# Kernel tuning notes

Measured on AMD Instinct MI355X. Metric: run time of the kernel, lower is better.

The kernel has to match this reference:

```python
import jax
import jax.numpy as jnp
from jax import lax
import numpy as np

B, T, C, L = 512, 512, 128, 80
BLANK = C - 1  # Keras ctc_batch_cost uses last class as blank
NEG = -1e30
EPS = 1e-7


def setup_inputs() -> dict:
    key = jax.random.key(0)
    k1, k2 = jax.random.split(key)
    # y_pred: positive "probability-like" activations, as ctc_batch_cost expects
    y_pred = jax.random.uniform(k1, (B, T, C), dtype=jnp.float32)
    # labels: non-blank symbols in [0, C-2]
    y_true = jax.random.randint(k2, (B, L), 0, C - 1, dtype=jnp.int64)
    return {"y_true": y_true, "y_pred": y_pred}


def _ctc_loss(log_probs, labels):
    """log_probs: [B,T,C] log-softmax; labels: [B,L] ints. Returns [B,1] loss."""
    b, t, c = log_probs.shape
    l = labels.shape[1]
    s = 2 * l + 1
    # extended label sequence: blank, l1, blank, l2, ..., blank  -> [B,S]
    ext = jnp.full((b, s), BLANK, dtype=labels.dtype).at[:, 1::2].set(labels)
    # per-time log-prob of each extended symbol: [B,T,S]
    lp = jnp.take_along_axis(log_probs, ext[:, None, :], axis=2)
    # skip-transition allowed where symbol is non-blank and differs from s-2
    ext_m2 = jnp.concatenate([jnp.full((b, 2), BLANK, ext.dtype), ext[:, :-2]], axis=1)
    allow2 = (ext != BLANK) & (ext != ext_m2)  # [B,S]

    alpha0 = (jnp.full((b, s), NEG, dtype=log_probs.dtype)
              .at[:, 0].set(lp[:, 0, 0])
              .at[:, 1].set(lp[:, 0, 1]))

    neg1 = jnp.full((b, 1), NEG, dtype=log_probs.dtype)
    neg2 = jnp.full((b, 2), NEG, dtype=log_probs.dtype)

    def step(alpha, lp_t):
        a1 = jnp.concatenate([neg1, alpha[:, :-1]], axis=1)
        a2 = jnp.concatenate([neg2, alpha[:, :-2]], axis=1)
        a2 = jnp.where(allow2, a2, NEG)
        m = jnp.maximum(jnp.maximum(alpha, a1), a2)
        lse = m + jnp.log(jnp.exp(alpha - m) + jnp.exp(a1 - m) + jnp.exp(a2 - m))
        return lp_t + lse, None

    lp_t_first = jnp.swapaxes(lp, 0, 1)  # [T,B,S]
    alphaT, _ = lax.scan(step, alpha0, lp_t_first[1:])
    loss = -jnp.logaddexp(alphaT[:, s - 1], alphaT[:, s - 2])  # [B]
    return loss[:, None]


def reference(y_true, y_pred):
    # K.ctc_batch_cost: log(y_pred + eps), then tf.nn.ctc_loss (softmax inside)
    log_probs = jax.nn.log_softmax(jnp.log(y_pred + EPS), axis=-1)
    return _ctc_loss(log_probs, y_true)
```

## Files before the change

kernel.cpp:

```cpp
#include <hip/hip_runtime.h>

#define B_ 512
#define T_ 512
#define C_ 128
#define L_ 80
#define BLANK_ 127
#define EPS_ 1e-7f
#define LN2_ 0.6931471805599453f

#define LOG2F(x) __builtin_amdgcn_logf(x)

template <int CTRL>
__device__ __forceinline__ int dpp_i(int x) {
  return __builtin_amdgcn_update_dpp(0, x, CTRL, 0xF, 0xF, true);
}
template <int CTRL>
__device__ __forceinline__ float dpp_f(float x) {
  return __int_as_float(
      __builtin_amdgcn_update_dpp(0, __float_as_int(x), CTRL, 0xF, 0xF, true));
}
#define DPP_WSHR1 0x138
#define DPP_XOR1  0xB1
#define DPP_XOR2  0x4E
#define DPP_HMIRR 0x141
#define DPP_MIRR  0x140

__global__ __launch_bounds__(64) void ctc_fused(
    const int* __restrict__ labels,
    const float* __restrict__ y_pred,
    float* __restrict__ out)
{
  const int b = blockIdx.x, lane = threadIdx.x;
  const float4* rp = (const float4*)(y_pred + (size_t)b * T_ * C_);
  __shared__ float ring[2 * 8 * C_];

  const int rgrp = lane >> 3, j16 = lane & 7;
  const bool evenLane = ((lane & 1) == 0);

  auto labAt = [&](int k) -> int {
    return (k >= 0 && k < L_) ? labels[b * L_ + k] : BLANK_;
  };
  int ea, eb;
  float m0, m1, m2;
  if (evenLane) {
    const int k1 = (3 * lane) >> 1;
    ea = labAt(k1); eb = ea;
    m0 = 0.f; m2 = 0.f;
    m1 = ((k1 < L_) && (k1 == 0 || ea != labAt(k1 - 1))) ? 1.f : 0.f;
  } else {
    const int k0 = (3 * lane - 1) >> 1;
    const int k2 = k0 + 1;
    ea = labAt(k0); eb = labAt(k2);
    m0 = ((k0 < L_) && (k0 == 0 || ea != labAt(k0 - 1))) ? 1.f : 0.f;
    m1 = 0.f;
    m2 = ((k2 < L_) && (eb != ea)) ? 1.f : 0.f;
  }

  float4 S0[4], S1[4], S2[4];
  {
    const float4* p0 = rp + (0 * 8 + rgrp) * 32 + 4 * j16;
    const float4* p1 = rp + (1 * 8 + rgrp) * 32 + 4 * j16;
    const float4* p2 = rp + (2 * 8 + rgrp) * 32 + 4 * j16;
    #pragma unroll
    for (int k = 0; k < 4; ++k) { S0[k] = p0[k]; S1[k] = p1[k]; S2[k] = p2[k]; }
  }

  float Sacc = 0.f;

  auto prep = [&](float4 (&Sw)[4], int bankDst) {
    #pragma unroll
    for (int k = 0; k < 4; ++k) {
      Sw[k].x += EPS_; Sw[k].y += EPS_; Sw[k].z += EPS_; Sw[k].w += EPS_;
    }
    float4* wd = (float4*)(ring + bankDst * 1024 + rgrp * C_ + 16 * j16);
    #pragma unroll
    for (int k = 0; k < 4; ++k) wd[k] = Sw[k];
    float s = 0.f;
    #pragma unroll
    for (int k = 0; k < 4; ++k)
      s += (Sw[k].x + Sw[k].y) + (Sw[k].z + Sw[k].w);
    s += dpp_f<DPP_XOR1>(s);
    s += dpp_f<DPP_XOR2>(s);
    s += dpp_f<DPP_HMIRR>(s);
    Sacc += LOG2F(s);
  };

  prep(S0, 0);

  float A0 = (lane == 0) ? 1.f : 0.f, A1 = 0.f, A2 = 0.f;
  int E = 0;
  float ga[8], gb[8], pb[8];

  auto body = [&](int n, float4 (&Sld)[4], float4 (&Swr)[4], bool doPrep) {
    const int bank = n & 1;
    const int EL = dpp_i<DPP_WSHR1>(E);
    const int d = E - EL;
    const float* rb = ring + bank * 1024;
    #pragma unroll
    for (int j = 0; j < 8; ++j) {
      ga[j] = rb[j * C_ + ea];
      gb[j] = rb[j * C_ + eb];
      pb[j] = rb[j * C_ + BLANK_];
    }
    {
      int r8 = (n + 3) * 8 + rgrp; if (r8 > T_ - 1) r8 = T_ - 1;
      const float4* src = rp + r8 * 32 + 4 * j16;
      #pragma unroll
      for (int k = 0; k < 4; ++k) Sld[k] = src[k];
    }
    if (doPrep) prep(Swr, bank ^ 1);
    #pragma unroll
    for (int j = 0; j < 8; ++j) {
      const float p1 = dpp_f<DPP_WSHR1>(A1);
      const float p2 = dpp_f<DPP_WSHR1>(A2);
      const float p1p = ldexpf(p1, d);
      const float p2p = ldexpf(p2, d);
      const float q0 = evenLane ? pb[j] : ga[j];
      const float q1 = evenLane ? ga[j] : pb[j];
      const float q2 = evenLane ? pb[j] : gb[j];
      const float t0 = q0 * fmaf(m0, p1p, A0 + p2p);
      const float t1 = q1 * fmaf(m1, p2p, A1 + A0);
      const float t2 = q2 * fmaf(m2, A0, A2 + A1);
      A0 = t0; A1 = t1; A2 = t2;
    }
    {
      const float mx = fmaxf(fmaxf(A0, A1), A2);
      int ee = (int)((__float_as_uint(mx) >> 23) & 255u) - 127;
      const bool z = (mx == 0.f);
      ee = z ? 0 : ee;
      A0 = ldexpf(A0, -ee); A1 = ldexpf(A1, -ee); A2 = ldexpf(A2, -ee);
      E = z ? EL : (E - ee);
    }
  };

  for (int nn = 0; nn < 63; nn += 3) {
    body(nn,     S0, S1, true);
    body(nn + 1, S1, S2, true);
    body(nn + 2, S2, S0, true);
  }
  body(63, S0, S1, false);

  float s = Sacc;
  s += dpp_f<DPP_XOR1>(s);
  s += dpp_f<DPP_XOR2>(s);
  s += dpp_f<DPP_HMIRR>(s);
  s += dpp_f<DPP_MIRR>(s);
  s += __shfl_xor(s, 16, 64);
  s += __shfl_xor(s, 32, 64);
  const float Stot = s * 0.125f;

  if (lane == 53) {
    const float lse2 = LOG2F(A0 + A1) - (float)E;
    out[b] = LN2_ * (Stot - lse2);
  }
}

extern "C" void kernel_launch(void* const* d_in, const int* in_sizes, int n_in,
                              void* d_out, int out_size, void* d_ws, size_t ws_size,
                              hipStream_t stream) {
  const int*   labels = (const int*)d_in[0];
  const float* y_pred = (const float*)d_in[1];
  float*       out    = (float*)d_out;
  ctc_fused<<<dim3(B_), dim3(64), 0, stream>>>(labels, y_pred, out);
}
```

Before: 192.3 us.

## Split CTC recursion into forward and backward halves with producer warps

Each batch block now runs four waves. Two consumer waves carry the alpha recursion forward over the first half of time and the beta recursion backward over the second half. Two producer waves load and normalize the y_pred rows into a shared ring, and the halves are combined by a scaled dot product at the midpoint. This halves the serial recursion length and takes the load and prep work off the critical wave. In exchange it adds a __syncthreads per 8-row block and a more involved combine step with exponent tracking.

```diff
diff --git a/kernel.cpp b/kernel.cpp
--- a/kernel.cpp
+++ b/kernel.cpp
@@ -7,6 +7,7 @@
 #define BLANK_ 127
 #define EPS_ 1e-7f
 #define LN2_ 0.6931471805599453f
+#define NBLK_ 32
 
 #define LOG2F(x) __builtin_amdgcn_logf(x)
 
@@ -20,138 +21,228 @@
       __builtin_amdgcn_update_dpp(0, __float_as_int(x), CTRL, 0xF, 0xF, true));
 }
 #define DPP_WSHR1 0x138
+#define DPP_WSHL1 0x130
 #define DPP_XOR1  0xB1
 #define DPP_XOR2  0x4E
 #define DPP_HMIRR 0x141
 #define DPP_MIRR  0x140
 
-__global__ __launch_bounds__(64) void ctc_fused(
+__global__ __launch_bounds__(256) void ctc_fused(
     const int* __restrict__ labels,
     const float* __restrict__ y_pred,
     float* __restrict__ out)
 {
-  const int b = blockIdx.x, lane = threadIdx.x;
-  const float4* rp = (const float4*)(y_pred + (size_t)b * T_ * C_);
-  __shared__ float ring[2 * 8 * C_];
-
+  const int b = blockIdx.x;
+  const int tid = threadIdx.x;
+  const int wid = tid >> 6;
+  const int lane = tid & 63;
+  const float* gp = y_pred + (size_t)b * T_ * C_;
+
+  __shared__ float ring[2 * 2 * 1024];
+  __shared__ float comb[208];
+  __shared__ int   combE[64];
+
+  const bool isCons = (wid < 2);
+  const bool isFwd  = (wid == 0);
+  const bool evenLane = ((lane & 1) == 0);
+
+  int ea = BLANK_, eb = BLANK_;
+  float m0 = 0.f, m1 = 0.f, m2 = 0.f;
+  float A0 = 0.f, A1 = 0.f, A2 = 0.f;
+  int E = 0;
+  if (isCons) {
+    auto labAt = [&](int k) -> int {
+      return (k >= 0 && k < L_) ? labels[b * L_ + k] : BLANK_;
+    };
+    if (evenLane) {
+      const int k1 = (3 * lane) >> 1;
+      ea = labAt(k1); eb = ea;
+      if (isFwd) {
+        m1 = ((k1 < L_) && (k1 == 0 || ea != labAt(k1 - 1))) ? 1.f : 0.f;
+      } else {
+        m1 = ((k1 + 1 < L_) && (labAt(k1 + 1) != ea)) ? 1.f : 0.f;
+      }
+    } else {
+      const int k0 = (3 * lane - 1) >> 1;
+      const int k2 = k0 + 1;
+      ea = labAt(k0); eb = labAt(k2);
+      if (isFwd) {
+        m0 = ((k0 < L_) && (k0 == 0 || ea != labAt(k0 - 1))) ? 1.f : 0.f;
+        m2 = ((k2 < L_) && (eb != ea)) ? 1.f : 0.f;
+      } else {
+        m0 = ((k2 < L_) && (eb != ea)) ? 1.f : 0.f;
+        m2 = ((k0 + 2 < L_) && (labAt(k0 + 2) != eb)) ? 1.f : 0.f;
+      }
+    }
+    if (isFwd) A0 = (lane == 0) ? 1.f : 0.f;
+    else       A1 = (lane == 53) ? 1.f : 0.f;
+  }
+
+  const int dir = wid & 1;
   const int rgrp = lane >> 3, j16 = lane & 7;
-  const bool evenLane = ((lane & 1) == 0);
-
-  auto labAt = [&](int k) -> int {
-    return (k >= 0 && k < L_) ? labels[b * L_ + k] : BLANK_;
-  };
-  int ea, eb;
-  float m0, m1, m2;
-  if (evenLane) {
-    const int k1 = (3 * lane) >> 1;
-    ea = labAt(k1); eb = ea;
-    m0 = 0.f; m2 = 0.f;
-    m1 = ((k1 < L_) && (k1 == 0 || ea != labAt(k1 - 1))) ? 1.f : 0.f;
-  } else {
-    const int k0 = (3 * lane - 1) >> 1;
-    const int k2 = k0 + 1;
-    ea = labAt(k0); eb = labAt(k2);
-    m0 = ((k0 < L_) && (k0 == 0 || ea != labAt(k0 - 1))) ? 1.f : 0.f;
-    m1 = 0.f;
-    m2 = ((k2 < L_) && (eb != ea)) ? 1.f : 0.f;
-  }
-
   float4 S0[4], S1[4], S2[4];
-  {
-    const float4* p0 = rp + (0 * 8 + rgrp) * 32 + 4 * j16;
-    const float4* p1 = rp + (1 * 8 + rgrp) * 32 + 4 * j16;
-    const float4* p2 = rp + (2 * 8 + rgrp) * 32 + 4 * j16;
-    #pragma unroll
-    for (int k = 0; k < 4; ++k) { S0[k] = p0[k]; S1[k] = p1[k]; S2[k] = p2[k]; }
-  }
-
   float Sacc = 0.f;
-
-  auto prep = [&](float4 (&Sw)[4], int bankDst) {
+  float* ringD = ring + dir * 2048;
+  const float* ringC = ring + wid * 2048;
+
+  auto rowbase = [&](int blk) -> const float4* {
+    const int r0 = dir ? (504 - 8 * blk) : (8 * blk);
+    return (const float4*)(gp + (size_t)(r0 + rgrp) * C_) + 4 * j16;
+  };
+  auto loadset = [&](float4 (&S)[4], int blk) {
+    const float4* p = rowbase(blk);
+    #pragma unroll
+    for (int k = 0; k < 4; ++k) S[k] = p[k];
+  };
+  auto prep = [&](float4 (&S)[4], int bank) {
     #pragma unroll
     for (int k = 0; k < 4; ++k) {
-      Sw[k].x += EPS_; Sw[k].y += EPS_; Sw[k].z += EPS_; Sw[k].w += EPS_;
-    }
-    float4* wd = (float4*)(ring + bankDst * 1024 + rgrp * C_ + 16 * j16);
-    #pragma unroll
-    for (int k = 0; k < 4; ++k) wd[k] = Sw[k];
+      S[k].x += EPS_; S[k].y += EPS_; S[k].z += EPS_; S[k].w += EPS_;
+    }
+    float4* wd = (float4*)(ringD + bank * 1024 + rgrp * C_ + 16 * j16);
+    #pragma unroll
+    for (int k = 0; k < 4; ++k) wd[k] = S[k];
     float s = 0.f;
     #pragma unroll
-    for (int k = 0; k < 4; ++k)
-      s += (Sw[k].x + Sw[k].y) + (Sw[k].z + Sw[k].w);
+    for (int k = 0; k < 4; ++k) s += (S[k].x + S[k].y) + (S[k].z + S[k].w);
     s += dpp_f<DPP_XOR1>(s);
     s += dpp_f<DPP_XOR2>(s);
     s += dpp_f<DPP_HMIRR>(s);
     Sacc += LOG2F(s);
   };
 
-  prep(S0, 0);
-
-  float A0 = (lane == 0) ? 1.f : 0.f, A1 = 0.f, A2 = 0.f;
-  int E = 0;
-  float ga[8], gb[8], pb[8];
-
-  auto body = [&](int n, float4 (&Sld)[4], float4 (&Swr)[4], bool doPrep) {
+  auto consume = [&](int n) {
     const int bank = n & 1;
-    const int EL = dpp_i<DPP_WSHR1>(E);
-    const int d = E - EL;
-    const float* rb = ring + bank * 1024;
-    #pragma unroll
-    for (int j = 0; j < 8; ++j) {
-      ga[j] = rb[j * C_ + ea];
-      gb[j] = rb[j * C_ + eb];
-      pb[j] = rb[j * C_ + BLANK_];
-    }
-    {
-      int r8 = (n + 3) * 8 + rgrp; if (r8 > T_ - 1) r8 = T_ - 1;
-      const float4* src = rp + r8 * 32 + 4 * j16;
-      #pragma unroll
-      for (int k = 0; k < 4; ++k) Sld[k] = src[k];
-    }
-    if (doPrep) prep(Swr, bank ^ 1);
-    #pragma unroll
-    for (int j = 0; j < 8; ++j) {
-      const float p1 = dpp_f<DPP_WSHR1>(A1);
-      const float p2 = dpp_f<DPP_WSHR1>(A2);
-      const float p1p = ldexpf(p1, d);
-      const float p2p = ldexpf(p2, d);
-      const float q0 = evenLane ? pb[j] : ga[j];
-      const float q1 = evenLane ? ga[j] : pb[j];
-      const float q2 = evenLane ? pb[j] : gb[j];
-      const float t0 = q0 * fmaf(m0, p1p, A0 + p2p);
-      const float t1 = q1 * fmaf(m1, p2p, A1 + A0);
-      const float t2 = q2 * fmaf(m2, A0, A2 + A1);
-      A0 = t0; A1 = t1; A2 = t2;
-    }
-    {
+    const float* rb = ringC + bank * 1024;
+    float ga[8], gb[8], pb[8];
+    if (isFwd) {
+      const int EL = dpp_i<DPP_WSHR1>(E);
+      const int d = E - EL;
+      #pragma unroll
+      for (int j = 0; j < 8; ++j) {
+        ga[j] = rb[j * C_ + ea];
+        gb[j] = rb[j * C_ + eb];
+        pb[j] = rb[j * C_ + BLANK_];
+      }
+      #pragma unroll
+      for (int j = 0; j < 8; ++j) {
+        const float p1 = dpp_f<DPP_WSHR1>(A1);
+        const float p2 = dpp_f<DPP_WSHR1>(A2);
+        const float p1p = ldexpf(p1, d);
+        const float p2p = ldexpf(p2, d);
+        const float q0 = evenLane ? pb[j] : ga[j];
+        const float q1 = evenLane ? ga[j] : pb[j];
+        const float q2 = evenLane ? pb[j] : gb[j];
+        const float t0 = q0 * fmaf(m0, p1p, A0 + p2p);
+        const float t1 = q1 * fmaf(m1, p2p, A1 + A0);
+        const float t2 = q2 * fmaf(m2, A0, A2 + A1);
+        A0 = t0; A1 = t1; A2 = t2;
+      }
       const float mx = fmaxf(fmaxf(A0, A1), A2);
       int ee = (int)((__float_as_uint(mx) >> 23) & 255u) - 127;
       const bool z = (mx == 0.f);
       ee = z ? 0 : ee;
       A0 = ldexpf(A0, -ee); A1 = ldexpf(A1, -ee); A2 = ldexpf(A2, -ee);
       E = z ? EL : (E - ee);
-    }
-  };
-
-  for (int nn = 0; nn < 63; nn += 3) {
-    body(nn,     S0, S1, true);
-    body(nn + 1, S1, S2, true);
-    body(nn + 2, S2, S0, true);
-  }
-  body(63, S0, S1, false);
-
-  float s = Sacc;
-  s += dpp_f<DPP_XOR1>(s);
-  s += dpp_f<DPP_XOR2>(s);
-  s += dpp_f<DPP_HMIRR>(s);
-  s += dpp_f<DPP_MIRR>(s);
-  s += __shfl_xor(s, 16, 64);
-  s += __shfl_xor(s, 32, 64);
-  const float Stot = s * 0.125f;
-
-  if (lane == 53) {
-    const float lse2 = LOG2F(A0 + A1) - (float)E;
-    out[b] = LN2_ * (Stot - lse2);
+    } else {
+      const int ER = dpp_i<DPP_WSHL1>(E);
+      const int d = E - ER;
+      #pragma unroll
+      for (int j = 0; j < 8; ++j) {
+        const int sl = 7 - j;
+        ga[j] = rb[sl * C_ + ea];
+        gb[j] = rb[sl * C_ + eb];
+        pb[j] = rb[sl * C_ + BLANK_];
+      }
+      #pragma unroll
+      for (int j = 0; j < 8; ++j) {
+        const float r0 = dpp_f<DPP_WSHL1>(A0);
+        const float r1 = dpp_f<DPP_WSHL1>(A1);
+        const float r0p = ldexpf(r0, d);
+        const float r1p = ldexpf(r1, d);
+        const float q0 = evenLane ? pb[j] : ga[j];
+        const float q1 = evenLane ? ga[j] : pb[j];
+        const float q2 = evenLane ? pb[j] : gb[j];
+        const float t0 = q0 * fmaf(m0, A2, A0 + A1);
+        const float t1 = q1 * fmaf(m1, r0p, A1 + A2);
+        const float t2 = q2 * fmaf(m2, r1p, A2 + r0p);
+        A0 = t0; A1 = t1; A2 = t2;
+      }
+      const float mx = fmaxf(fmaxf(A0, A1), A2);
+      int ee = (int)((__float_as_uint(mx) >> 23) & 255u) - 127;
+      const bool z = (mx == 0.f);
+      ee = z ? 0 : ee;
+      A0 = ldexpf(A0, -ee); A1 = ldexpf(A1, -ee); A2 = ldexpf(A2, -ee);
+      E = z ? ER : (E - ee);
+    }
+  };
+
+  if (!isCons) {
+    loadset(S0, 0); loadset(S1, 1); loadset(S2, 2);
+    prep(S0, 0);
+    loadset(S0, 3);
+  }
+  __syncthreads();
+
+  for (int n = 0; n < 30; n += 3) {
+    { if (isCons) consume(n);
+      else { prep(S1, (n + 1) & 1); if (n + 4 < NBLK_) loadset(S1, n + 4); } }
+    __syncthreads();
+    { if (isCons) consume(n + 1);
+      else { prep(S2, (n + 2) & 1); if (n + 5 < NBLK_) loadset(S2, n + 5); } }
+    __syncthreads();
+    { if (isCons) consume(n + 2);
+      else { prep(S0, (n + 3) & 1); if (n + 6 < NBLK_) loadset(S0, n + 6); } }
+    __syncthreads();
+  }
+  { if (isCons) consume(30); else prep(S1, 1); }
+  __syncthreads();
+  if (isCons) consume(31);
+  __syncthreads();
+
+  if (wid == 1) {
+    const int ER = dpp_i<DPP_WSHL1>(E);
+    const int d = E - ER;
+    const float r0 = dpp_f<DPP_WSHL1>(A0);
+    const float r1 = dpp_f<DPP_WSHL1>(A1);
+    const float r0p = ldexpf(r0, d);
+    const float r1p = ldexpf(r1, d);
+    comb[3 * lane + 0] = fmaf(m0, A2, A0 + A1);
+    comb[3 * lane + 1] = fmaf(m1, r0p, A1 + A2);
+    comb[3 * lane + 2] = fmaf(m2, r1p, A2 + r0p);
+    combE[lane] = E;
+  } else if (wid >= 2) {
+    float s = Sacc;
+    s += dpp_f<DPP_XOR1>(s);
+    s += dpp_f<DPP_XOR2>(s);
+    s += dpp_f<DPP_HMIRR>(s);
+    s += dpp_f<DPP_MIRR>(s);
+    s += __shfl_xor(s, 16, 64);
+    s += __shfl_xor(s, 32, 64);
+    if (lane == 0) comb[200 + dir] = s * 0.125f;
+  }
+  __syncthreads();
+
+  if (wid == 0) {
+    const float b0 = comb[3 * lane + 0];
+    const float b1 = comb[3 * lane + 1];
+    const float b2 = comb[3 * lane + 2];
+    const int   EB = combE[lane];
+    float v = A0 * b0 + A1 * b1 + A2 * b2;
+    int e = -(E + EB);
+    if (v == 0.f) e = -100000000;
+    #pragma unroll
+    for (int off = 1; off < 64; off <<= 1) {
+      const float v2 = __shfl_xor(v, off, 64);
+      const int   e2 = __shfl_xor(e, off, 64);
+      const int m = (e > e2) ? e : e2;
+      v = ldexpf(v, e - m) + ldexpf(v2, e2 - m);
+      e = m;
+    }
+    if (lane == 0) {
+      const float Stot = comb[200] + comb[201];
+      out[b] = LN2_ * (Stot - (LOG2F(v) + (float)e));
+    }
   }
 }
 
@@ -161,5 +252,5 @@
   const int*   labels = (const int*)d_in[0];
   const float* y_pred = (const float*)d_in[1];
   float*       out    = (float*)d_out;
-  ctc_fused<<<dim3(B_), dim3(64), 0, stream>>>(labels, y_pred, out);
-}
+  ctc_fused<<<dim3(B_), dim3(256), 0, stream>>>(labels, y_pred, out);
+}
```

Measured after the change: 192.2 us. No clear change (-0.1%).

## Warp-specialize CTC kernel: one recurrence wave, three producer waves staging LDS

Applied to the files above, without the earlier changes.

Splits each block into four waves. Wave 0 runs only the alpha recurrence, two 8-timestep blocks per iteration. The other three waves take turns loading global rows, adding eps, writing a 4-bank LDS ring, and accumulating log row sums. The aim is to take global-load latency and preprocessing off the serial recurrence's critical path. The cost is a block-wide __syncthreads every 16 timesteps, 4x the threads per block, and more LDS.

```diff
diff --git a/kernel.cpp b/kernel.cpp
--- a/kernel.cpp
+++ b/kernel.cpp
@@ -25,133 +25,150 @@
 #define DPP_HMIRR 0x141
 #define DPP_MIRR  0x140
 
-__global__ __launch_bounds__(64) void ctc_fused(
+__global__ __launch_bounds__(256) void ctc_fused(
     const int* __restrict__ labels,
     const float* __restrict__ y_pred,
     float* __restrict__ out)
 {
-  const int b = blockIdx.x, lane = threadIdx.x;
-  const float4* rp = (const float4*)(y_pred + (size_t)b * T_ * C_);
-  __shared__ float ring[2 * 8 * C_];
+  const int b = blockIdx.x, tid = threadIdx.x;
+  const int wid = tid >> 6, lane = tid & 63;
+  const float* gp = y_pred + (size_t)b * T_ * C_;
+
+  __shared__ float ring[4 * 1024];
+  __shared__ float comb[4];
+
+  const bool evenLane = ((lane & 1) == 0);
+
+  int ea = BLANK_, eb = BLANK_;
+  float m0 = 0.f, m1 = 0.f, m2 = 0.f;
+  float A0 = 0.f, A1 = 0.f, A2 = 0.f;
+  int E = 0;
+  if (wid == 0) {
+    auto labAt = [&](int k) -> int {
+      return (k >= 0 && k < L_) ? labels[b * L_ + k] : BLANK_;
+    };
+    if (evenLane) {
+      const int k1 = (3 * lane) >> 1;
+      ea = labAt(k1); eb = ea;
+      m1 = ((k1 < L_) && (k1 == 0 || ea != labAt(k1 - 1))) ? 1.f : 0.f;
+    } else {
+      const int k0 = (3 * lane - 1) >> 1;
+      const int k2 = k0 + 1;
+      ea = labAt(k0); eb = labAt(k2);
+      m0 = ((k0 < L_) && (k0 == 0 || ea != labAt(k0 - 1))) ? 1.f : 0.f;
+      m2 = ((k2 < L_) && (eb != ea)) ? 1.f : 0.f;
+    }
+    A0 = (lane == 0) ? 1.f : 0.f;
+  }
 
   const int rgrp = lane >> 3, j16 = lane & 7;
-  const bool evenLane = ((lane & 1) == 0);
-
-  auto labAt = [&](int k) -> int {
-    return (k >= 0 && k < L_) ? labels[b * L_ + k] : BLANK_;
-  };
-  int ea, eb;
-  float m0, m1, m2;
-  if (evenLane) {
-    const int k1 = (3 * lane) >> 1;
-    ea = labAt(k1); eb = ea;
-    m0 = 0.f; m2 = 0.f;
-    m1 = ((k1 < L_) && (k1 == 0 || ea != labAt(k1 - 1))) ? 1.f : 0.f;
-  } else {
-    const int k0 = (3 * lane - 1) >> 1;
-    const int k2 = k0 + 1;
-    ea = labAt(k0); eb = labAt(k2);
-    m0 = ((k0 < L_) && (k0 == 0 || ea != labAt(k0 - 1))) ? 1.f : 0.f;
-    m1 = 0.f;
-    m2 = ((k2 < L_) && (eb != ea)) ? 1.f : 0.f;
-  }
-
-  float4 S0[4], S1[4], S2[4];
-  {
-    const float4* p0 = rp + (0 * 8 + rgrp) * 32 + 4 * j16;
-    const float4* p1 = rp + (1 * 8 + rgrp) * 32 + 4 * j16;
-    const float4* p2 = rp + (2 * 8 + rgrp) * 32 + 4 * j16;
-    #pragma unroll
-    for (int k = 0; k < 4; ++k) { S0[k] = p0[k]; S1[k] = p1[k]; S2[k] = p2[k]; }
-  }
-
+  float4 SA[8];
   float Sacc = 0.f;
 
-  auto prep = [&](float4 (&Sw)[4], int bankDst) {
+  auto loadpair = [&](int P) {
     #pragma unroll
-    for (int k = 0; k < 4; ++k) {
-      Sw[k].x += EPS_; Sw[k].y += EPS_; Sw[k].z += EPS_; Sw[k].w += EPS_;
+    for (int h = 0; h < 2; ++h) {
+      const float4* src =
+          (const float4*)(gp + (size_t)(16 * P + 8 * h + rgrp) * C_) + 4 * j16;
+      #pragma unroll
+      for (int k = 0; k < 4; ++k) SA[4 * h + k] = src[k];
     }
-    float4* wd = (float4*)(ring + bankDst * 1024 + rgrp * C_ + 16 * j16);
+  };
+  auto preppair = [&](int P) {
     #pragma unroll
-    for (int k = 0; k < 4; ++k) wd[k] = Sw[k];
-    float s = 0.f;
-    #pragma unroll
-    for (int k = 0; k < 4; ++k)
-      s += (Sw[k].x + Sw[k].y) + (Sw[k].z + Sw[k].w);
-    s += dpp_f<DPP_XOR1>(s);
-    s += dpp_f<DPP_XOR2>(s);
-    s += dpp_f<DPP_HMIRR>(s);
-    Sacc += LOG2F(s);
+    for (int h = 0; h < 2; ++h) {
+      const int blk = 2 * P + h;
+      float4* wd = (float4*)(ring + (blk & 3) * 1024 + rgrp * C_ + 16 * j16);
+      float s = 0.f;
+      #pragma unroll
+      for (int k = 0; k < 4; ++k) {
+        float4 v = SA[4 * h + k];
+        v.x += EPS_; v.y += EPS_; v.z += EPS_; v.w += EPS_;
+        wd[k] = v;
+        s += (v.x + v.y) + (v.z + v.w);
+      }
+      s += dpp_f<DPP_XOR1>(s);
+      s += dpp_f<DPP_XOR2>(s);
+      s += dpp_f<DPP_HMIRR>(s);
+      Sacc += LOG2F(s);
+    }
   };
 
-  prep(S0, 0);
-
-  float A0 = (lane == 0) ? 1.f : 0.f, A1 = 0.f, A2 = 0.f;
-  int E = 0;
-  float ga[8], gb[8], pb[8];
-
-  auto body = [&](int n, float4 (&Sld)[4], float4 (&Swr)[4], bool doPrep) {
-    const int bank = n & 1;
+  auto stepBlock = [&](const float* g, const float* h, const float* p) {
     const int EL = dpp_i<DPP_WSHR1>(E);
     const int d = E - EL;
-    const float* rb = ring + bank * 1024;
-    #pragma unroll
-    for (int j = 0; j < 8; ++j) {
-      ga[j] = rb[j * C_ + ea];
-      gb[j] = rb[j * C_ + eb];
-      pb[j] = rb[j * C_ + BLANK_];
-    }
-    {
-      int r8 = (n + 3) * 8 + rgrp; if (r8 > T_ - 1) r8 = T_ - 1;
-      const float4* src = rp + r8 * 32 + 4 * j16;
-      #pragma unroll
-      for (int k = 0; k < 4; ++k) Sld[k] = src[k];
-    }
-    if (doPrep) prep(Swr, bank ^ 1);
     #pragma unroll
     for (int j = 0; j < 8; ++j) {
       const float p1 = dpp_f<DPP_WSHR1>(A1);
       const float p2 = dpp_f<DPP_WSHR1>(A2);
       const float p1p = ldexpf(p1, d);
       const float p2p = ldexpf(p2, d);
-      const float q0 = evenLane ? pb[j] : ga[j];
-      const float q1 = evenLane ? ga[j] : pb[j];
-      const float q2 = evenLane ? pb[j] : gb[j];
+      const float q0 = evenLane ? p[j] : g[j];
+      const float q1 = evenLane ? g[j] : p[j];
+      const float q2 = evenLane ? p[j] : h[j];
       const float t0 = q0 * fmaf(m0, p1p, A0 + p2p);
       const float t1 = q1 * fmaf(m1, p2p, A1 + A0);
       const float t2 = q2 * fmaf(m2, A0, A2 + A1);
       A0 = t0; A1 = t1; A2 = t2;
     }
-    {
-      const float mx = fmaxf(fmaxf(A0, A1), A2);
-      int ee = (int)((__float_as_uint(mx) >> 23) & 255u) - 127;
-      const bool z = (mx == 0.f);
-      ee = z ? 0 : ee;
-      A0 = ldexpf(A0, -ee); A1 = ldexpf(A1, -ee); A2 = ldexpf(A2, -ee);
-      E = z ? EL : (E - ee);
-    }
+    const float mx = fmaxf(fmaxf(A0, A1), A2);
+    int ee = (int)((__float_as_uint(mx) >> 23) & 255u) - 127;
+    const bool z = (mx == 0.f);
+    ee = z ? 0 : ee;
+    A0 = ldexpf(A0, -ee); A1 = ldexpf(A1, -ee); A2 = ldexpf(A2, -ee);
+    E = z ? EL : (E - ee);
   };
 
-  for (int nn = 0; nn < 63; nn += 3) {
-    body(nn,     S0, S1, true);
-    body(nn + 1, S1, S2, true);
-    body(nn + 2, S2, S0, true);
+  if (wid != 0) {
+    loadpair(wid - 1);
+    if (wid == 1) { preppair(0); loadpair(3); }
   }
-  body(63, S0, S1, false);
+  __syncthreads();
 
-  float s = Sacc;
-  s += dpp_f<DPP_XOR1>(s);
-  s += dpp_f<DPP_XOR2>(s);
-  s += dpp_f<DPP_HMIRR>(s);
-  s += dpp_f<DPP_MIRR>(s);
-  s += __shfl_xor(s, 16, 64);
-  s += __shfl_xor(s, 32, 64);
-  const float Stot = s * 0.125f;
+  for (int k = 0; k < 32; ++k) {
+    if (wid == 0) {
+      const float* rb0 = ring + ((2 * k) & 3) * 1024;
+      const float* rb1 = ring + ((2 * k + 1) & 3) * 1024;
+      float gA[8], hA[8], pA[8], gB[8], hB[8], pB[8];
+      #pragma unroll
+      for (int j = 0; j < 8; ++j) {
+        gA[j] = rb0[j * C_ + ea];
+        hA[j] = rb0[j * C_ + eb];
+        pA[j] = rb0[j * C_ + BLANK_];
+      }
+      #pragma unroll
+      for (int j = 0; j < 8; ++j) {
+        gB[j] = rb1[j * C_ + ea];
+        hB[j] = rb1[j * C_ + eb];
+        pB[j] = rb1[j * C_ + BLANK_];
+      }
+      stepBlock(gA, hA, pA);
+      stepBlock(gB, hB, pB);
+    } else {
+      const int P = k + 1;
+      if (P < 32 && (P % 3) == (wid - 1)) {
+        preppair(P);
+        if (P + 3 < 32) loadpair(P + 3);
+      }
+    }
+    __syncthreads();
+  }
 
-  if (lane == 53) {
-    const float lse2 = LOG2F(A0 + A1) - (float)E;
-    out[b] = LN2_ * (Stot - lse2);
+  if (wid != 0) {
+    float s = Sacc;
+    s += dpp_f<DPP_XOR1>(s);
+    s += dpp_f<DPP_XOR2>(s);
+    s += dpp_f<DPP_HMIRR>(s);
+    s += dpp_f<DPP_MIRR>(s);
+    s += __shfl_xor(s, 16, 64);
+    s += __shfl_xor(s, 32, 64);
+    if (lane == 0) comb[wid] = s * 0.125f;
+  }
+  __syncthreads();
+
+  if (wid == 0 && lane == 53) {
+    const float Stot = comb[1] + comb[2] + comb[3];
+    out[b] = LN2_ * (Stot - (LOG2F(A0 + A1) - (float)E));
   }
 }
 
@@ -161,5 +178,5 @@
   const int*   labels = (const int*)d_in[0];
   const float* y_pred = (const float*)d_in[1];
   float*       out    = (float*)d_out;
-  ctc_fused<<<dim3(B_), dim3(64), 0, stream>>>(labels, y_pred, out);
+  ctc_fused<<<dim3(B_), dim3(256), 0, stream>>>(labels, y_pred, out);
 }
```

After: 194.3 us. About the same (+1.0%).
